# Kernel tuning notes

Measured on AMD Instinct MI355X. Metric: run time of the kernel, lower is better.

Reference implementation:

```python
import jax, jax.numpy as jnp
import numpy as np

HIDDEN_DIM = 64
VOCAB_SIZE = 64
MEMORY_SLOTS = 4
SEQ_LEN = 48
B = 524288


def setup_inputs() -> dict:
    key = jax.random.key(0)
    ks = jax.random.split(key, 6)
    seqs = jax.random.randint(ks[0], (B, SEQ_LEN), 0, VOCAB_SIZE, dtype=jnp.int64 if jax.config.jax_enable_x64 else jnp.int32)
    query_tok = jax.random.randint(ks[1], (B,), 0, VOCAB_SIZE, dtype=seqs.dtype)
    embed = jax.random.normal(ks[2], (VOCAB_SIZE + 2, HIDDEN_DIM), dtype=jnp.float32) * 0.02
    W1 = jax.random.normal(ks[3], (HIDDEN_DIM, HIDDEN_DIM * 2), dtype=jnp.float32) * 0.05
    b1 = jnp.zeros((HIDDEN_DIM,), dtype=jnp.float32)
    W2 = jax.random.normal(ks[4], (VOCAB_SIZE, HIDDEN_DIM), dtype=jnp.float32) * 0.05
    b2 = jnp.zeros((VOCAB_SIZE,), dtype=jnp.float32)
    return {"seqs": seqs, "query_tok": query_tok, "embed": embed,
            "W1": W1, "b1": b1, "W2": W2, "b2": b2}


def reference(seqs, query_tok, embed, W1, b1, W2, b2):
    # FIFO of size MEMORY_SLOTS over tokens t=0..SEQ_LEN-2 == last MEMORY_SLOTS of them
    mem_tok = seqs[:, SEQ_LEN - 1 - MEMORY_SLOTS:SEQ_LEN - 1]      # [B, MEMORY_SLOTS]
    mem_summary = embed[mem_tok].mean(axis=1)                       # [B, H]
    q_emb = embed[query_tok]                                        # [B, H]
    x = jnp.concatenate([q_emb, mem_summary], axis=-1)              # [B, 2H]
    h = jax.nn.relu(x @ W1.T + b1)                                  # [B, H]
    return h @ W2.T + b2                                            # [B, VOCAB]
```

## Files before the change

### kernel.cpp

```cpp
#include <hip/hip_runtime.h>
#include <hip/hip_bf16.h>

#define HD 64
#define VOCAB 64
#define SEQ 48
#define MEMSLOTS 4
#define TSTRIDE 66

using frag_ab = __attribute__((ext_vector_type(8))) short;
using frag_cd = __attribute__((ext_vector_type(4))) float;
typedef __attribute__((ext_vector_type(4))) float floatx4;

static __device__ inline unsigned short f2bf(float f) {
  unsigned u = __float_as_uint(f);
  unsigned r = (u + 0x7fffu + ((u >> 16) & 1u)) >> 16;
  return (unsigned short)r;
}

__global__ void build_tables(const float* __restrict__ embed,
                             const float* __restrict__ W1,
                             const float* __restrict__ b1,
                             float* __restrict__ T) {
  int v = blockIdx.x;
  int j = threadIdx.x;
  const float* e = embed + v * HD;
  const float* w1r = W1 + j * (2 * HD);
  float s1 = 0.f, s2 = 0.f;
  for (int k = 0; k < HD; ++k) {
    float ev = e[k];
    s1 += ev * w1r[k];
    s2 += ev * w1r[HD + k];
  }
  T[v * TSTRIDE + j] = s1 + b1[j];
  T[VOCAB * TSTRIDE + v * TSTRIDE + j] = 0.25f * s2;
}

__global__ __launch_bounds__(256, 4) void lru_main(
    const int* __restrict__ seqs, const int* __restrict__ qtok,
    const float* __restrict__ W2, const float* __restrict__ b2,
    const float* __restrict__ T, float* __restrict__ out, int nbatch) {
  __shared__ float sT[2 * VOCAB * TSTRIDE];

  {
    const floatx4* src = (const floatx4*)T;
    floatx4* dst = (floatx4*)sT;
    const int n4 = 2 * VOCAB * TSTRIDE / 4;
    for (int i = threadIdx.x; i < n4; i += blockDim.x) dst[i] = src[i];
  }
  __syncthreads();

  const int lane = threadIdx.x & 63;
  const int quad = lane >> 4;
  const int m    = lane & 15;
  const int k0   = quad * 8;

  frag_ab bf[4][2];
  for (int t = 0; t < 4; ++t)
    for (int s = 0; s < 2; ++s) {
      const float* w2r = W2 + (t * 16 + m) * HD + s * 32 + k0;
      for (int j = 0; j < 8; ++j) bf[t][s][j] = (short)f2bf(w2r[j]);
    }
  float b2v[4];
  for (int t = 0; t < 4; ++t) b2v[t] = b2[t * 16 + m];

  const int wave = blockIdx.x * (blockDim.x >> 6) + (threadIdx.x >> 6);
  const int nw   = gridDim.x * (blockDim.x >> 6);

  const float* T1 = sT;
  const float* T2 = sT + VOCAB * TSTRIDE;

  for (int b = wave; b < nbatch; b += nw) {
    const int rb  = b * 16;
    const int row = rb + m;
    const int q   = qtok[row];
    const int* sp = seqs + row * SEQ;
    const int ta  = sp[43];
    const int4 tb = *(const int4*)(sp + 44);

    float2 a[8];
    {
      const float2* p1  = (const float2*)(T1 + q * TSTRIDE + k0);
      const float2* p1b = (const float2*)(T1 + q * TSTRIDE + 32 + k0);
      for (int c = 0; c < 4; ++c) { a[c] = p1[c]; a[4 + c] = p1b[c]; }
      const int toks[4] = {ta, tb.x, tb.y, tb.z};
      for (int u = 0; u < 4; ++u) {
        const float2* p2  = (const float2*)(T2 + toks[u] * TSTRIDE + k0);
        const float2* p2b = (const float2*)(T2 + toks[u] * TSTRIDE + 32 + k0);
        for (int c = 0; c < 4; ++c) {
          float2 x = p2[c], y = p2b[c];
          a[c].x += x.x; a[c].y += x.y;
          a[4 + c].x += y.x; a[4 + c].y += y.y;
        }
      }
    }

    frag_ab a0, a1;
    for (int c = 0; c < 4; ++c) {
      a0[2 * c]     = (short)f2bf(fmaxf(a[c].x, 0.f));
      a0[2 * c + 1] = (short)f2bf(fmaxf(a[c].y, 0.f));
      a1[2 * c]     = (short)f2bf(fmaxf(a[4 + c].x, 0.f));
      a1[2 * c + 1] = (short)f2bf(fmaxf(a[4 + c].y, 0.f));
    }

    frag_cd acc[4];
    for (int t = 0; t < 4; ++t) {
      acc[t] = (frag_cd){0.f, 0.f, 0.f, 0.f};
      acc[t] = __builtin_amdgcn_mfma_f32_16x16x32_bf16(a0, bf[t][0], acc[t], 0, 0, 0);
      acc[t] = __builtin_amdgcn_mfma_f32_16x16x32_bf16(a1, bf[t][1], acc[t], 0, 0, 0);
    }

    float* orow = out + (size_t)rb * HD;
    for (int t = 0; t < 4; ++t)
      for (int p = 0; p < 4; ++p)
        orow[(quad * 4 + p) * HD + t * 16 + m] = acc[t][p] + b2v[t];
  }
}

extern "C" void kernel_launch(void* const* d_in, const int* in_sizes, int n_in,
                              void* d_out, int out_size, void* d_ws, size_t ws_size,
                              hipStream_t stream) {
  const int*   seqs  = (const int*)d_in[0];
  const int*   qtok  = (const int*)d_in[1];
  const float* embed = (const float*)d_in[2];
  const float* W1    = (const float*)d_in[3];
  const float* b1    = (const float*)d_in[4];
  const float* W2    = (const float*)d_in[5];
  const float* b2    = (const float*)d_in[6];
  float* out = (float*)d_out;
  float* T   = (float*)d_ws;

  const int B = in_sizes[1];
  const int nbatch = B / 16;

  build_tables<<<VOCAB, HD, 0, stream>>>(embed, W1, b1, T);
  lru_main<<<2048, 256, 0, stream>>>(seqs, qtok, W2, b2, T, out, nbatch);
}
```

Baseline: 237.9 us.

## Prefetch token indices one group ahead, distribute via shuffles, nontemporal stores

Each lane now loads the token indices for one row of a 64-row group, and they are handed out to 16-row MFMA tiles with wave shuffles. The loads for the next group are issued before the current group is computed, and the first group's loads are hoisted ahead of the shared-table copy. Output writes use nontemporal stores and the grid is halved. The aim is to hide the latency of the scattered seqs and qtok gathers and to cut cache pollution from the large output stream. In exchange, each wave holds more live registers and there are fewer waves to hide latency.

```diff
diff --git a/kernel.cpp b/kernel.cpp
--- a/kernel.cpp
+++ b/kernel.cpp
@@ -1,10 +1,8 @@
 #include <hip/hip_runtime.h>
-#include <hip/hip_bf16.h>
 
 #define HD 64
 #define VOCAB 64
 #define SEQ 48
-#define MEMSLOTS 4
 #define TSTRIDE 66
 
 using frag_ab = __attribute__((ext_vector_type(8))) short;
@@ -39,7 +37,28 @@
     const int* __restrict__ seqs, const int* __restrict__ qtok,
     const float* __restrict__ W2, const float* __restrict__ b2,
     const float* __restrict__ T, float* __restrict__ out, int nbatch) {
-  __shared__ float sT[2 * VOCAB * TSTRIDE];
+  __shared__ __align__(16) float sT[2 * VOCAB * TSTRIDE];
+
+  const int lane = threadIdx.x & 63;
+  const int quad = lane >> 4;
+  const int m    = lane & 15;
+  const int k0   = quad * 8;
+
+  const int wave = blockIdx.x * (blockDim.x >> 6) + (threadIdx.x >> 6);
+  const int nw   = gridDim.x * (blockDim.x >> 6);
+  const int R    = nbatch * 16;
+  const int ngroup = (nbatch + 3) >> 2;
+
+  int g = wave;
+  int q_cur = 0, a_cur = 0;
+  int4 b_cur = make_int4(0, 0, 0, 0);
+  if (g < ngroup) {
+    int r = g * 64 + lane; if (r >= R) r = R - 1;
+    q_cur = qtok[r];
+    const int* sp = seqs + (size_t)r * SEQ;
+    a_cur = sp[43];
+    b_cur = *(const int4*)(sp + 44);
+  }
 
   {
     const floatx4* src = (const floatx4*)T;
@@ -48,11 +67,6 @@
     for (int i = threadIdx.x; i < n4; i += blockDim.x) dst[i] = src[i];
   }
   __syncthreads();
-
-  const int lane = threadIdx.x & 63;
-  const int quad = lane >> 4;
-  const int m    = lane & 15;
-  const int k0   = quad * 8;
 
   frag_ab bf[4][2];
   for (int t = 0; t < 4; ++t)
@@ -63,56 +77,73 @@
   float b2v[4];
   for (int t = 0; t < 4; ++t) b2v[t] = b2[t * 16 + m];
 
-  const int wave = blockIdx.x * (blockDim.x >> 6) + (threadIdx.x >> 6);
-  const int nw   = gridDim.x * (blockDim.x >> 6);
-
   const float* T1 = sT;
   const float* T2 = sT + VOCAB * TSTRIDE;
 
-  for (int b = wave; b < nbatch; b += nw) {
-    const int rb  = b * 16;
-    const int row = rb + m;
-    const int q   = qtok[row];
-    const int* sp = seqs + row * SEQ;
-    const int ta  = sp[43];
-    const int4 tb = *(const int4*)(sp + 44);
+  for (; g < ngroup; g += nw) {
+    const int gn = g + nw;
+    int q_nxt = 0, a_nxt = 0;
+    int4 b_nxt = make_int4(0, 0, 0, 0);
+    if (gn < ngroup) {
+      int r = gn * 64 + lane; if (r >= R) r = R - 1;
+      q_nxt = qtok[r];
+      const int* sp = seqs + (size_t)r * SEQ;
+      a_nxt = sp[43];
+      b_nxt = *(const int4*)(sp + 44);
+    }
 
-    float2 a[8];
-    {
-      const float2* p1  = (const float2*)(T1 + q * TSTRIDE + k0);
-      const float2* p1b = (const float2*)(T1 + q * TSTRIDE + 32 + k0);
-      for (int c = 0; c < 4; ++c) { a[c] = p1[c]; a[4 + c] = p1b[c]; }
-      const int toks[4] = {ta, tb.x, tb.y, tb.z};
-      for (int u = 0; u < 4; ++u) {
-        const float2* p2  = (const float2*)(T2 + toks[u] * TSTRIDE + k0);
-        const float2* p2b = (const float2*)(T2 + toks[u] * TSTRIDE + 32 + k0);
-        for (int c = 0; c < 4; ++c) {
-          float2 x = p2[c], y = p2b[c];
-          a[c].x += x.x; a[c].y += x.y;
-          a[4 + c].x += y.x; a[4 + c].y += y.y;
+#pragma unroll
+    for (int it = 0; it < 4; ++it) {
+      const int b = g * 4 + it;
+      if (b >= nbatch) break;
+
+      const int src = it * 16 + m;
+      const int q  = __shfl(q_cur, src);
+      const int t0 = __shfl(a_cur, src);
+      const int t1 = __shfl(b_cur.x, src);
+      const int t2 = __shfl(b_cur.y, src);
+      const int t3 = __shfl(b_cur.z, src);
+
+      float2 a[8];
+      {
+        const float2* p1  = (const float2*)(T1 + q * TSTRIDE + k0);
+        const float2* p1b = (const float2*)(T1 + q * TSTRIDE + 32 + k0);
+        for (int c = 0; c < 4; ++c) { a[c] = p1[c]; a[4 + c] = p1b[c]; }
+        const int toks[4] = {t0, t1, t2, t3};
+        for (int u = 0; u < 4; ++u) {
+          const float2* p2  = (const float2*)(T2 + toks[u] * TSTRIDE + k0);
+          const float2* p2b = (const float2*)(T2 + toks[u] * TSTRIDE + 32 + k0);
+          for (int c = 0; c < 4; ++c) {
+            float2 x = p2[c], y = p2b[c];
+            a[c].x += x.x; a[c].y += x.y;
+            a[4 + c].x += y.x; a[4 + c].y += y.y;
+          }
         }
       }
+
+      frag_ab a0, a1;
+      for (int c = 0; c < 4; ++c) {
+        a0[2 * c]     = (short)f2bf(fmaxf(a[c].x, 0.f));
+        a0[2 * c + 1] = (short)f2bf(fmaxf(a[c].y, 0.f));
+        a1[2 * c]     = (short)f2bf(fmaxf(a[4 + c].x, 0.f));
+        a1[2 * c + 1] = (short)f2bf(fmaxf(a[4 + c].y, 0.f));
+      }
+
+      frag_cd acc[4];
+      for (int t = 0; t < 4; ++t) {
+        acc[t] = (frag_cd){0.f, 0.f, 0.f, 0.f};
+        acc[t] = __builtin_amdgcn_mfma_f32_16x16x32_bf16(a0, bf[t][0], acc[t], 0, 0, 0);
+        acc[t] = __builtin_amdgcn_mfma_f32_16x16x32_bf16(a1, bf[t][1], acc[t], 0, 0, 0);
+      }
+
+      float* orow = out + (size_t)(b * 16) * HD;
+      for (int t = 0; t < 4; ++t)
+        for (int p = 0; p < 4; ++p)
+          __builtin_nontemporal_store(acc[t][p] + b2v[t],
+                                      &orow[(quad * 4 + p) * HD + t * 16 + m]);
     }
 
-    frag_ab a0, a1;
-    for (int c = 0; c < 4; ++c) {
-      a0[2 * c]     = (short)f2bf(fmaxf(a[c].x, 0.f));
-      a0[2 * c + 1] = (short)f2bf(fmaxf(a[c].y, 0.f));
-      a1[2 * c]     = (short)f2bf(fmaxf(a[4 + c].x, 0.f));
-      a1[2 * c + 1] = (short)f2bf(fmaxf(a[4 + c].y, 0.f));
-    }
-
-    frag_cd acc[4];
-    for (int t = 0; t < 4; ++t) {
-      acc[t] = (frag_cd){0.f, 0.f, 0.f, 0.f};
-      acc[t] = __builtin_amdgcn_mfma_f32_16x16x32_bf16(a0, bf[t][0], acc[t], 0, 0, 0);
-      acc[t] = __builtin_amdgcn_mfma_f32_16x16x32_bf16(a1, bf[t][1], acc[t], 0, 0, 0);
-    }
-
-    float* orow = out + (size_t)rb * HD;
-    for (int t = 0; t < 4; ++t)
-      for (int p = 0; p < 4; ++p)
-        orow[(quad * 4 + p) * HD + t * 16 + m] = acc[t][p] + b2v[t];
+    q_cur = q_nxt; a_cur = a_nxt; b_cur = b_nxt;
   }
 }
 
@@ -133,5 +164,5 @@
   const int nbatch = B / 16;
 
   build_tables<<<VOCAB, HD, 0, stream>>>(embed, W1, b1, T);
-  lru_main<<<2048, 256, 0, stream>>>(seqs, qtok, W2, b2, T, out, nbatch);
+  lru_main<<<1024, 256, 0, stream>>>(seqs, qtok, W2, b2, T, out, nbatch);
 }
```

After: 239.2 us. No clear change (+0.5%).
